# Optimization experiments

Hardware: AMD Instinct MI355X
Metric: run time of the kernel (lower is better)

## Reference

```python
import jax, jax.numpy as jnp
import numpy as np

N_CLUSTER = 1
SIZE, RATIO = 32, 0.1


def _lin_mat(n_in, n_out):
    # bilinear, align_corners=True interpolation matrix [n_out, n_in]
    src = np.arange(n_out) * (n_in - 1) / (n_out - 1)
    lo = np.floor(src).astype(np.int64)
    hi = np.minimum(lo + 1, n_in - 1)
    w = (src - lo).astype(np.float32)
    M = np.zeros((n_out, n_in), np.float32)
    M[np.arange(n_out), lo] += 1.0 - w
    M[np.arange(n_out), hi] += w
    return jnp.asarray(M)


def setup_inputs() -> dict:
    key = jax.random.key(0)
    ks = jax.random.split(key, 5)
    B, D, H, W, C = 16, 128, 128, 128, 6
    inp = {
        "assp": jax.random.normal(ks[0], (B, D, H, W), jnp.float32),
        "cls_w": jax.random.normal(ks[1], (C, D), jnp.float32) * 0.05,
        "cls_b": jnp.zeros((C,), jnp.float32),
        "key_w": jax.random.normal(ks[2], (128, D), jnp.float32) * 0.05,
        "key_b": jnp.zeros((128,), jnp.float32),
        "query_w": jax.random.normal(ks[3], (C, 128, D), jnp.float32) * 0.05,
        "query_b": jnp.zeros((C, 128), jnp.float32),
    }
    rng = np.random.default_rng(0)
    idx = rng.permutation(SIZE * SIZE)[: int(SIZE * SIZE * RATIO)]  # 102 unique pixels
    inp["px"] = jnp.asarray(idx // SIZE, jnp.int32)
    inp["py"] = jnp.asarray(idx % SIZE, jnp.int32)
    return inp


def reference(assp, cls_w, cls_b, key_w, key_b, query_w, query_b, px, py):
    B, D, H, W = assp.shape
    C = cls_w.shape[0]
    # pseudo labels (torch.no_grad)
    feats = jax.lax.stop_gradient(assp)
    pseudo = jnp.einsum('bdhw,cd->bchw', feats, cls_w) + cls_b[None, :, None, None]
    mask = jnp.argmax(pseudo, axis=1)                      # [B,H,W]
    onehot = jax.nn.one_hot(mask, C, dtype=assp.dtype)      # [B,H,W,C]
    counts = onehot.sum((1, 2))                             # [B,C]
    sums = jnp.einsum('bdhw,bhwc->bcd', assp, onehot)       # masked class sums
    protoC = sums / (counts[..., None] + 1e-5)              # [B,C,D]
    protoC = jnp.where(counts[..., None] > 0, protoC, 0.0)  # zero_prototype fallback
    protos12 = jnp.broadcast_to(protoC[:, :, None, :], (B, C, 2, D)).reshape(B, 2 * C, D)

    # DomainTrain: gather sampled pixels, L2 dist to 12 prototypes, argmin, scatter replace
    feat_px = assp[:, :, px, py]                            # [B,D,Np]
    diff = protos12[:, :, None, :] - feat_px.transpose(0, 2, 1)[:, None, :, :]  # [B,12,Np,D]
    dist = jnp.linalg.norm(diff, axis=-1)                   # [B,12,Np]
    closest = jnp.argmin(dist, axis=1)                      # [B,Np]
    repl = jnp.take_along_axis(protos12, closest[..., None], axis=1)  # [B,Np,D]
    assp = assp.at[:, :, px, py].set(repl.transpose(0, 2, 1))
    protos4 = protos12.reshape(B, C, 2, D)

    # key / query attention
    keymap = jnp.einsum('bdhw,kd->bkhw', assp, key_w) + key_b[None, :, None, None]
    q = jnp.einsum('bijd,ikd->bijk', protos4, query_w) + query_b[None, :, None, :]  # [B,C,2,128]
    sim = jnp.einsum('bijk,bkhw->bijhw', q, keymap).reshape(B, 2 * C, H, W)
    simw = jax.nn.softmax(sim / (2 * C) * N_CLUSTER, axis=1).mean(axis=1)  # [B,H,W]

    weighted = assp * simw[:, None]
    x = jnp.einsum('bdhw,cd->bchw', weighted, cls_w) + cls_b[None, :, None, None]
    My = _lin_mat(H, 4 * H)
    Mx = _lin_mat(W, 4 * W)
    xup = jnp.einsum('Hh,bchw,Ww->bcHW', My, x, Mx)
    return xup
```

## Files before the change

kernel.cpp:

```cpp
#include <hip/hip_runtime.h>

namespace {

constexpr int B  = 16;
constexpr int D  = 128;
constexpr int C  = 6;
constexpr int H  = 128;
constexpr int W  = 128;
constexpr int HWC = H * W;
constexpr int HO = 512, WO = 512;
constexpr int CHUNK = 2048;

__global__ __launch_bounds__(256) void k_cls(const float* __restrict__ assp,
                                             const float* __restrict__ cls_w,
                                             const float* __restrict__ cls_b,
                                             float* __restrict__ x,
                                             unsigned char* __restrict__ mask,
                                             int* __restrict__ counts) {
  __shared__ int csh[4 * C];

  const int t  = threadIdx.x;
  const int b  = blockIdx.y;
  const int px = blockIdx.x * 256 + t;
  const int lane = t & 63;
  const int wv   = t >> 6;

  const float* col = assp + ((size_t)b * D) * HWC + px;

  float a[C] = {0.f, 0.f, 0.f, 0.f, 0.f, 0.f};
#pragma unroll 8
  for (int d = 0; d < D; ++d) {
    float vv = col[(size_t)d * HWC];
#pragma unroll
    for (int c = 0; c < C; ++c) a[c] += vv * cls_w[c * D + d];
  }

  float bv = a[0] + cls_b[0];
  int cls = 0;
#pragma unroll
  for (int c = 1; c < C; ++c) {
    float pv = a[c] + cls_b[c];
    if (pv > bv) { bv = pv; cls = c; }
  }

  const float inv12 = 1.0f / 12.0f;
  float* xb = x + ((size_t)b * C) * HWC + px;
#pragma unroll
  for (int c = 0; c < C; ++c) xb[(size_t)c * HWC] = a[c] * inv12 + cls_b[c];

  mask[(size_t)b * HWC + px] = (unsigned char)cls;

#pragma unroll
  for (int c = 0; c < C; ++c) {
    unsigned long long m = __ballot(cls == c);
    if (lane == 0) csh[wv * C + c] = (int)__popcll(m);
  }
  __syncthreads();
  if (t < C)
    atomicAdd(&counts[b * C + t],
              csh[0 * C + t] + csh[1 * C + t] + csh[2 * C + t] + csh[3 * C + t]);
}

__global__ __launch_bounds__(256) void k_sum(const float* __restrict__ assp,
                                             const unsigned char* __restrict__ mask,
                                             float* __restrict__ sums) {
  const int t    = threadIdx.x;
  const int lane = t & 63;
  const int wv   = t >> 6;
  const int b    = blockIdx.z;
  const int d    = blockIdx.y * 4 + wv;
  const int px0  = blockIdx.x * CHUNK;

  const float* row = assp + ((size_t)b * D + d) * HWC + px0;
  const unsigned char* mrow = mask + (size_t)b * HWC + px0;

  float acc[C] = {0.f, 0.f, 0.f, 0.f, 0.f, 0.f};
#pragma unroll 4
  for (int i = 0; i < CHUNK / 64; ++i) {
    float vv = row[i * 64 + lane];
    int   c  = mrow[i * 64 + lane];
#pragma unroll
    for (int cc = 0; cc < C; ++cc) acc[cc] += (c == cc) ? vv : 0.f;
  }

  float out = 0.f;
#pragma unroll
  for (int cc = 0; cc < C; ++cc) {
    float s = acc[cc];
#pragma unroll
    for (int off = 32; off >= 1; off >>= 1) s += __shfl_xor(s, off, 64);
    if (lane == cc) out = s;
  }
  if (lane < C) atomicAdd(&sums[((size_t)b * C + lane) * D + d], out);
}

__global__ void k_patch(const float* __restrict__ assp,
                        const float* __restrict__ sums,
                        const int* __restrict__ counts,
                        const float* __restrict__ cls_w,
                        const float* __restrict__ cls_b,
                        const int* __restrict__ px,
                        const int* __restrict__ py,
                        int P,
                        float* __restrict__ x) {
  int bp = blockIdx.x;
  int b = bp / P, p = bp % P;
  int hw = px[p] * W + py[p];
  int lane = threadIdx.x;
  const float* fbase = assp + ((size_t)b * D) * HWC + hw;

  float f0 = fbase[(size_t)lane * HWC];
  float f1 = fbase[(size_t)(lane + 64) * HWC];

  float pv0[C], pv1[C], ds[C];
#pragma unroll
  for (int c = 0; c < C; ++c) {
    float cnt = (float)counts[b * C + c];
    float s0 = sums[((size_t)b * C + c) * D + lane];
    float s1 = sums[((size_t)b * C + c) * D + lane + 64];
    float q0 = (cnt > 0.f) ? s0 / (cnt + 1e-5f) : 0.f;
    float q1 = (cnt > 0.f) ? s1 / (cnt + 1e-5f) : 0.f;
    pv0[c] = q0; pv1[c] = q1;
    float e0 = q0 - f0, e1 = q1 - f1;
    float tt = e0 * e0 + e1 * e1;
#pragma unroll
    for (int off = 32; off >= 1; off >>= 1) tt += __shfl_xor(tt, off, 64);
    ds[c] = tt;
  }
  int best = 0; float bv = ds[0];
#pragma unroll
  for (int c = 1; c < C; ++c)
    if (ds[c] < bv) { bv = ds[c]; best = c; }

  float v0 = 0.f, v1 = 0.f;
#pragma unroll
  for (int c = 0; c < C; ++c) {
    if (best == c) { v0 = pv0[c]; v1 = pv1[c]; }
  }

  float myx = 0.f;
#pragma unroll
  for (int c = 0; c < C; ++c) {
    float tt = v0 * cls_w[c * D + lane] + v1 * cls_w[c * D + lane + 64];
#pragma unroll
    for (int off = 32; off >= 1; off >>= 1) tt += __shfl_xor(tt, off, 64);
    float val = tt * (1.0f / 12.0f) + cls_b[c];
    if (lane == c) myx = val;
  }
  if (lane < C) x[((size_t)b * C + lane) * HWC + hw] = myx;
}

__global__ __launch_bounds__(256) void k_up(const float* __restrict__ x,
                                            float* __restrict__ out) {
  __shared__ float rows[3 * W];

  const int t = threadIdx.x;
  const size_t base = (size_t)blockIdx.x * 1024;
  const int bc = (int)(base >> 18);
  const int Y0 = ((int)(base >> 9)) & (HO - 1);

  const int ry = (Y0 * (H - 1)) / (HO - 1);

  if (t < 96) {
    int r  = t >> 5;
    int xx = (t & 31) * 4;
    int rr = ry + r; if (rr > H - 1) rr = H - 1;
    *(float4*)&rows[r * W + xx] =
        *(const float4*)(x + (size_t)bc * HWC + (size_t)rr * W + xx);
  }
  __syncthreads();

  const int h  = t >> 7;
  const int tt = t & 127;
  const int Y  = Y0 + h;

  const int ynum = Y * (H - 1);
  const int yl   = ynum / (HO - 1);
  const float wy = (float)((double)(ynum - yl * (HO - 1)) * (1.0 / (HO - 1)));
  int yh = yl + 1; if (yh > H - 1) yh = H - 1;
  const float* r0 = &rows[(yl - ry) * W];
  const float* r1 = &rows[(yh - ry) * W];

  float o[4];
#pragma unroll
  for (int j = 0; j < 4; ++j) {
    int X   = 4 * tt + j;
    int num = X * (W - 1);
    int lo  = num / (WO - 1);
    float wx = (float)((double)(num - lo * (WO - 1)) * (1.0 / (WO - 1)));
    int hi = lo + 1; if (hi > W - 1) hi = W - 1;

    float v00 = r0[lo], v01 = r0[hi], v10 = r1[lo], v11 = r1[hi];
    o[j] = (1.f - wy) * ((1.f - wx) * v00 + wx * v01)
         +        wy  * ((1.f - wx) * v10 + wx * v11);
  }
  float4 o4 = {o[0], o[1], o[2], o[3]};
  *(float4*)(out + base + (size_t)h * WO + 4 * tt) = o4;
}

}

extern "C" void kernel_launch(void* const* d_in, const int* in_sizes, int n_in,
                              void* d_out, int out_size, void* d_ws, size_t ws_size,
                              hipStream_t stream) {
  const float* assp  = (const float*)d_in[0];
  const float* cls_w = (const float*)d_in[1];
  const float* cls_b = (const float*)d_in[2];
  const int*   px    = (const int*)d_in[7];
  const int*   py    = (const int*)d_in[8];
  const int    P     = in_sizes[7];

  char* ws = (char*)d_ws;
  float* sums            = (float*)ws;
  int*   counts          = (int*)(ws + 49152);
  float* x               = (float*)(ws + 65536);
  unsigned char* maskbuf = (unsigned char*)(ws + 8388608);

  float* out = (float*)d_out;

  hipMemsetAsync(ws, 0, 49152 + 384, stream);
  k_cls<<<dim3(HWC / 256, B), 256, 0, stream>>>(assp, cls_w, cls_b, x, maskbuf, counts);
  k_sum<<<dim3(HWC / CHUNK, D / 4, B), 256, 0, stream>>>(assp, maskbuf, sums);
  k_patch<<<B * P, 64, 0, stream>>>(assp, sums, counts, cls_w, cls_b, px, py, P, x);
  k_up<<<(B * C * HO * WO) / 1024, 256, 0, stream>>>(x, out);
}
```

Measured before the change: 279.9 us.

## Fuse classification and masked class-sum kernels into one pass over assp

Merges the per-pixel classifier kernel and the masked prototype-sum kernel into a single kernel. Each wave reuses the class labels it just computed through lane shuffles and re-reads its 64-pixel strip of all 128 channels right away, while it is likely still in cache, instead of running a second full pass over assp and going through a byte mask buffer. Per-block partial sums are reduced in shared memory before global atomics, and per-wave count atomics replace the block-level count reduction. The cost is many more sum atomics per block (768 per block across 1024 blocks), a 12 KB shared buffer that may limit occupancy, and a strided float4 access pattern across channels in the second phase.

```diff
diff --git a/kernel.cpp b/kernel.cpp
--- a/kernel.cpp
+++ b/kernel.cpp
@@ -9,24 +9,23 @@
 constexpr int W  = 128;
 constexpr int HWC = H * W;
 constexpr int HO = 512, WO = 512;
-constexpr int CHUNK = 2048;
-
-__global__ __launch_bounds__(256) void k_cls(const float* __restrict__ assp,
-                                             const float* __restrict__ cls_w,
-                                             const float* __restrict__ cls_b,
-                                             float* __restrict__ x,
-                                             unsigned char* __restrict__ mask,
-                                             int* __restrict__ counts) {
-  __shared__ int csh[4 * C];
-
-  const int t  = threadIdx.x;
-  const int b  = blockIdx.y;
-  const int px = blockIdx.x * 256 + t;
+
+__global__ __launch_bounds__(256) void k_fused(const float* __restrict__ assp,
+                                               const float* __restrict__ cls_w,
+                                               const float* __restrict__ cls_b,
+                                               float* __restrict__ sums,
+                                               int* __restrict__ counts,
+                                               float* __restrict__ x) {
+  __shared__ float part[4 * C * D];
+
+  const int t    = threadIdx.x;
+  const int b    = blockIdx.y;
   const int lane = t & 63;
   const int wv   = t >> 6;
+  const int px   = blockIdx.x * 256 + t;
+  const int px0  = blockIdx.x * 256 + wv * 64;
 
   const float* col = assp + ((size_t)b * D) * HWC + px;
-
   float a[C] = {0.f, 0.f, 0.f, 0.f, 0.f, 0.f};
 #pragma unroll 8
   for (int d = 0; d < D; ++d) {
@@ -48,50 +47,44 @@
 #pragma unroll
   for (int c = 0; c < C; ++c) xb[(size_t)c * HWC] = a[c] * inv12 + cls_b[c];
 
-  mask[(size_t)b * HWC + px] = (unsigned char)cls;
-
+  int cnt = 0;
 #pragma unroll
   for (int c = 0; c < C; ++c) {
     unsigned long long m = __ballot(cls == c);
-    if (lane == 0) csh[wv * C + c] = (int)__popcll(m);
+    if (lane == c) cnt = (int)__popcll(m);
+  }
+  if (lane < C) atomicAdd(&counts[b * C + lane], cnt);
+
+  const float* row0 = assp + ((size_t)b * D + lane) * HWC + px0;
+  const float* row1 = assp + ((size_t)b * D + lane + 64) * HWC + px0;
+  float acc0[C] = {0.f, 0.f, 0.f, 0.f, 0.f, 0.f};
+  float acc1[C] = {0.f, 0.f, 0.f, 0.f, 0.f, 0.f};
+#pragma unroll
+  for (int g = 0; g < 16; ++g) {
+    float4 u  = *(const float4*)(row0 + 4 * g);
+    float4 w4 = *(const float4*)(row1 + 4 * g);
+#pragma unroll
+    for (int j = 0; j < 4; ++j) {
+      int cj = __shfl(cls, 4 * g + j, 64);
+      float uj = (&u.x)[j];
+      float wj = (&w4.x)[j];
+#pragma unroll
+      for (int cc = 0; cc < C; ++cc)
+        if (cj == cc) { acc0[cc] += uj; acc1[cc] += wj; }
+    }
+  }
+
+#pragma unroll
+  for (int cc = 0; cc < C; ++cc) {
+    part[(wv * C + cc) * D + lane]      = acc0[cc];
+    part[(wv * C + cc) * D + lane + 64] = acc1[cc];
   }
   __syncthreads();
-  if (t < C)
-    atomicAdd(&counts[b * C + t],
-              csh[0 * C + t] + csh[1 * C + t] + csh[2 * C + t] + csh[3 * C + t]);
-}
-
-__global__ __launch_bounds__(256) void k_sum(const float* __restrict__ assp,
-                                             const unsigned char* __restrict__ mask,
-                                             float* __restrict__ sums) {
-  const int t    = threadIdx.x;
-  const int lane = t & 63;
-  const int wv   = t >> 6;
-  const int b    = blockIdx.z;
-  const int d    = blockIdx.y * 4 + wv;
-  const int px0  = blockIdx.x * CHUNK;
-
-  const float* row = assp + ((size_t)b * D + d) * HWC + px0;
-  const unsigned char* mrow = mask + (size_t)b * HWC + px0;
-
-  float acc[C] = {0.f, 0.f, 0.f, 0.f, 0.f, 0.f};
-#pragma unroll 4
-  for (int i = 0; i < CHUNK / 64; ++i) {
-    float vv = row[i * 64 + lane];
-    int   c  = mrow[i * 64 + lane];
-#pragma unroll
-    for (int cc = 0; cc < C; ++cc) acc[cc] += (c == cc) ? vv : 0.f;
-  }
-
-  float out = 0.f;
-#pragma unroll
-  for (int cc = 0; cc < C; ++cc) {
-    float s = acc[cc];
-#pragma unroll
-    for (int off = 32; off >= 1; off >>= 1) s += __shfl_xor(s, off, 64);
-    if (lane == cc) out = s;
-  }
-  if (lane < C) atomicAdd(&sums[((size_t)b * C + lane) * D + d], out);
+  for (int i = t; i < C * D; i += 256) {
+    float s = part[0 * C * D + i] + part[1 * C * D + i]
+            + part[2 * C * D + i] + part[3 * C * D + i];
+    atomicAdd(&sums[(size_t)b * C * D + i], s);
+  }
 }
 
 __global__ void k_patch(const float* __restrict__ assp,
@@ -211,16 +204,14 @@
   const int    P     = in_sizes[7];
 
   char* ws = (char*)d_ws;
-  float* sums            = (float*)ws;
-  int*   counts          = (int*)(ws + 49152);
-  float* x               = (float*)(ws + 65536);
-  unsigned char* maskbuf = (unsigned char*)(ws + 8388608);
+  float* sums   = (float*)ws;
+  int*   counts = (int*)(ws + 49152);
+  float* x      = (float*)(ws + 65536);
 
   float* out = (float*)d_out;
 
   hipMemsetAsync(ws, 0, 49152 + 384, stream);
-  k_cls<<<dim3(HWC / 256, B), 256, 0, stream>>>(assp, cls_w, cls_b, x, maskbuf, counts);
-  k_sum<<<dim3(HWC / CHUNK, D / 4, B), 256, 0, stream>>>(assp, maskbuf, sums);
+  k_fused<<<dim3(HWC / 256, B), 256, 0, stream>>>(assp, cls_w, cls_b, sums, counts, x);
   k_patch<<<B * P, 64, 0, stream>>>(assp, sums, counts, cls_w, cls_b, px, py, P, x);
   k_up<<<(B * C * HO * WO) / 1024, 256, 0, stream>>>(x, out);
 }
```

New measurement: 299.7 us. +7.1%, slower.

## Stage k_cls loads through LDS with float4 prefetch; vectorize k_sum with larger chunks

Applied to the files above, without the earlier changes.

k_cls now loads 32-channel slabs of the pixel block with float4 loads into shared memory, prefetching the next slab into registers while computing on the current one. The aim is wider loads and more memory-level parallelism than the old per-thread strided scalar loop. The per-block count reduction is replaced by per-wave atomics, which adds more atomics on counts. k_sum switches to float4/uchar4 loads over 8192-pixel chunks, so fewer blocks each do more work and fewer atomics are issued on sums, at the cost of less parallelism.

```diff
diff --git a/kernel.cpp b/kernel.cpp
--- a/kernel.cpp
+++ b/kernel.cpp
@@ -9,7 +9,6 @@
 constexpr int W  = 128;
 constexpr int HWC = H * W;
 constexpr int HO = 512, WO = 512;
-constexpr int CHUNK = 2048;
 
 __global__ __launch_bounds__(256) void k_cls(const float* __restrict__ assp,
                                              const float* __restrict__ cls_w,
@@ -17,22 +16,45 @@
                                              float* __restrict__ x,
                                              unsigned char* __restrict__ mask,
                                              int* __restrict__ counts) {
-  __shared__ int csh[4 * C];
-
-  const int t  = threadIdx.x;
-  const int b  = blockIdx.y;
-  const int px = blockIdx.x * 256 + t;
+  __shared__ float tile[32 * 256];
+
+  const int t    = threadIdx.x;
+  const int b    = blockIdx.y;
   const int lane = t & 63;
   const int wv   = t >> 6;
-
-  const float* col = assp + ((size_t)b * D) * HWC + px;
+  const int px0  = blockIdx.x * 256;
+  const int px   = px0 + t;
+
+  const float* bbase = assp + ((size_t)b * D) * HWC + px0;
+
+  float4 v[8];
+#pragma unroll
+  for (int r = 0; r < 8; ++r)
+    v[r] = *(const float4*)(bbase + (size_t)(wv * 8 + r) * HWC + lane * 4);
 
   float a[C] = {0.f, 0.f, 0.f, 0.f, 0.f, 0.f};
-#pragma unroll 8
-  for (int d = 0; d < D; ++d) {
-    float vv = col[(size_t)d * HWC];
-#pragma unroll
-    for (int c = 0; c < C; ++c) a[c] += vv * cls_w[c * D + d];
+
+  for (int ds = 0; ds < 4; ++ds) {
+#pragma unroll
+    for (int r = 0; r < 8; ++r)
+      *(float4*)&tile[(wv * 8 + r) * 256 + lane * 4] = v[r];
+    __syncthreads();
+
+    if (ds < 3) {
+      const float* nb = bbase + (size_t)((ds + 1) * 32) * HWC;
+#pragma unroll
+      for (int r = 0; r < 8; ++r)
+        v[r] = *(const float4*)(nb + (size_t)(wv * 8 + r) * HWC + lane * 4);
+    }
+
+#pragma unroll
+    for (int dd = 0; dd < 32; ++dd) {
+      float vv = tile[dd * 256 + t];
+      int d = ds * 32 + dd;
+#pragma unroll
+      for (int c = 0; c < C; ++c) a[c] += vv * cls_w[c * D + d];
+    }
+    __syncthreads();
   }
 
   float bv = a[0] + cls_b[0];
@@ -50,15 +72,13 @@
 
   mask[(size_t)b * HWC + px] = (unsigned char)cls;
 
+  int cnt = 0;
 #pragma unroll
   for (int c = 0; c < C; ++c) {
     unsigned long long m = __ballot(cls == c);
-    if (lane == 0) csh[wv * C + c] = (int)__popcll(m);
-  }
-  __syncthreads();
-  if (t < C)
-    atomicAdd(&counts[b * C + t],
-              csh[0 * C + t] + csh[1 * C + t] + csh[2 * C + t] + csh[3 * C + t]);
+    if (lane == c) cnt = (int)__popcll(m);
+  }
+  if (lane < C) atomicAdd(&counts[b * C + lane], cnt);
 }
 
 __global__ __launch_bounds__(256) void k_sum(const float* __restrict__ assp,
@@ -69,18 +89,23 @@
   const int wv   = t >> 6;
   const int b    = blockIdx.z;
   const int d    = blockIdx.y * 4 + wv;
-  const int px0  = blockIdx.x * CHUNK;
+  const int px0  = blockIdx.x * 8192;
 
   const float* row = assp + ((size_t)b * D + d) * HWC + px0;
   const unsigned char* mrow = mask + (size_t)b * HWC + px0;
 
   float acc[C] = {0.f, 0.f, 0.f, 0.f, 0.f, 0.f};
-#pragma unroll 4
-  for (int i = 0; i < CHUNK / 64; ++i) {
-    float vv = row[i * 64 + lane];
-    int   c  = mrow[i * 64 + lane];
-#pragma unroll
-    for (int cc = 0; cc < C; ++cc) acc[cc] += (c == cc) ? vv : 0.f;
+#pragma unroll 8
+  for (int i = 0; i < 32; ++i) {
+    float4 vv = *(const float4*)(row + i * 256 + lane * 4);
+    uchar4 mm = *(const uchar4*)(mrow + i * 256 + lane * 4);
+#pragma unroll
+    for (int cc = 0; cc < C; ++cc) {
+      acc[cc] += (mm.x == cc) ? vv.x : 0.f;
+      acc[cc] += (mm.y == cc) ? vv.y : 0.f;
+      acc[cc] += (mm.z == cc) ? vv.z : 0.f;
+      acc[cc] += (mm.w == cc) ? vv.w : 0.f;
+    }
   }
 
   float out = 0.f;
@@ -220,7 +245,7 @@
 
   hipMemsetAsync(ws, 0, 49152 + 384, stream);
   k_cls<<<dim3(HWC / 256, B), 256, 0, stream>>>(assp, cls_w, cls_b, x, maskbuf, counts);
-  k_sum<<<dim3(HWC / CHUNK, D / 4, B), 256, 0, stream>>>(assp, maskbuf, sums);
+  k_sum<<<dim3(HWC / 8192, D / 4, B), 256, 0, stream>>>(assp, maskbuf, sums);
   k_patch<<<B * P, 64, 0, stream>>>(assp, sums, counts, cls_w, cls_b, px, py, P, x);
   k_up<<<(B * C * HO * WO) / 1024, 256, 0, stream>>>(x, out);
 }
```

Result: slower. 305.3 us (+9.1%).
